# Performance work log

Hardware: AMD Instinct MI355X
Metric: run time of the kernel (lower is better)

Reference implementation:

```python
import jax, jax.numpy as jnp
import numpy as np

C = 512  # in_channels

def _maxpool2x2(t):
    # t: [B, c, H, W] -> [B, c, H//2, W//2]
    B, c, H, W = t.shape
    return t.reshape(B, c, H // 2, 2, W // 2, 2).max(axis=(3, 5))

def setup_inputs() -> dict:
    key = jax.random.key(0)
    ks = jax.random.split(key, 6)
    B, H, W = 16, 64, 64
    x = jax.random.normal(ks[0], (B, C, H, W), dtype=jnp.float32)
    # 1x1 conv weights (spectral norm is just a static rescale of the weight;
    # we model the post-normalized weight directly). Shapes: [out_c, in_c].
    scale = 0.02
    w_theta = jax.random.normal(ks[1], (C // 8, C), dtype=jnp.float32) * scale
    w_phi = jax.random.normal(ks[2], (C // 8, C), dtype=jnp.float32) * scale
    w_g = jax.random.normal(ks[3], (C // 2, C), dtype=jnp.float32) * scale
    w_o = jax.random.normal(ks[4], (C, C // 2), dtype=jnp.float32) * scale
    gamma = jnp.asarray(0.5, dtype=jnp.float32)  # nonzero so attention path matters
    return {"x": x, "w_theta": w_theta, "w_phi": w_phi, "w_g": w_g,
            "w_o": w_o, "gamma": gamma}

def reference(x, w_theta, w_phi, w_g, w_o, gamma):
    B, c, H, W = x.shape
    N = H * W
    M = N // 4
    # 1x1 convs == channel matmuls
    theta = jnp.einsum('oc,bchw->bohw', w_theta, x)            # [B, C/8, H, W]
    phi = _maxpool2x2(jnp.einsum('oc,bchw->bohw', w_phi, x))   # [B, C/8, H/2, W/2]
    g = _maxpool2x2(jnp.einsum('oc,bchw->bohw', w_g, x))       # [B, C/2, H/2, W/2]
    theta = theta.reshape(B, c // 8, N)
    phi = phi.reshape(B, c // 8, M)
    g = g.reshape(B, c // 2, M)
    # attention: softmax over keys (last dim)
    scores = jnp.einsum('bdn,bdm->bnm', theta, phi)            # [B, N, M]
    beta = jax.nn.softmax(scores, axis=-1)
    o = jnp.einsum('bvm,bnm->bvn', g, beta)                    # [B, C/2, N]
    o = o.reshape(B, c // 2, H, W)
    o = jnp.einsum('ov,bvhw->bohw', w_o, o)                    # [B, C, H, W]
    return gamma * o + x
```

## Files before the change

kernel.cpp:

```cpp
#include <hip/hip_runtime.h>
#include <hip/hip_fp16.h>

typedef unsigned int u32;
typedef unsigned short u16;
typedef u32 __attribute__((may_alias)) u32a;
typedef u16 __attribute__((may_alias)) u16a;
typedef uint4 __attribute__((may_alias)) uint4a;
typedef uint2 __attribute__((may_alias)) uint2a;
typedef float __attribute__((may_alias)) f32a;
typedef float4 __attribute__((may_alias)) float4a;

typedef __attribute__((ext_vector_type(8))) short short8v;
typedef __attribute__((ext_vector_type(4))) float float4v;

union Frag { uint4 q; short8v s; u16 u[8]; };
union F4 { float4 v; float f[4]; };

#define BATCH 16
#define CIN   512
#define NPIX  4096
#define DD    64
#define VV    256
#define MM    1024

__device__ __forceinline__ float b2f(u16 u) {
  union { u32 i; float f; } v; v.i = ((u32)u) << 16; return v.f;
}
__device__ __forceinline__ u16 f2b(float f) {
  union { float f; u32 i; } v; v.f = f;
  u32 u = v.i;
  u32 r = (u + 0x7fffu + ((u >> 16) & 1u)) >> 16;
  return (u16)r;
}
__device__ __forceinline__ u16 f2h(float f) { return __half_as_ushort(__float2half(f)); }
__device__ __forceinline__ float h2f(u16 u) { return __half2float(__ushort_as_half(u)); }

__device__ __forceinline__ u32 cvtpk(float lo, float hi) {
  u32 r;
  asm("v_cvt_pk_bf16_f32 %0, %1, %2" : "=v"(r) : "v"(lo), "v"(hi));
  return r;
}

__device__ __forceinline__ float dot2(u32 a, u32 b, float c) {
  union { u32 i; float f; } a0, a1, b0, b1;
  a0.i = a << 16; a1.i = a & 0xffff0000u;
  b0.i = b << 16; b1.i = b & 0xffff0000u;
  return fmaf(a1.f, b1.f, fmaf(a0.f, b0.f, c));
}

__global__ __launch_bounds__(256) void k_detect(const void* __restrict__ x,
                                                u32* __restrict__ meta) {
  __shared__ int bad[256];
  const int t = threadIdx.x;
  float f = b2f(((const u16a*)x)[2 * t]);
  float a = fabsf(f);
  bad[t] = (a >= 1e-6f && a <= 100.f) ? 0 : 1;
  __syncthreads();
  if (t == 0) {
    int s = 0;
#pragma unroll 16
    for (int i = 0; i < 256; ++i) s += bad[i];
    meta[0] = (s > 64) ? 1u : 0u;
  }
}

__global__ __launch_bounds__(256) void k_cvt(
    const void* __restrict__ wt, const void* __restrict__ wp,
    const void* __restrict__ wg, const void* __restrict__ wo,
    const void* __restrict__ gm, const u32* __restrict__ meta,
    u16* __restrict__ wbf, float* __restrict__ gout) {
  const int flag = (int)meta[0];
  const int i = blockIdx.x * 256 + threadIdx.x;
  const void* src; int j;
  if (i < 32768)       { src = wt; j = i; }
  else if (i < 65536)  { src = wp; j = i - 32768; }
  else if (i < 196608) { src = wg; j = i - 65536; }
  else                 { src = wo; j = i - 196608; }
  wbf[i] = flag ? f2b(((const f32a*)src)[j]) : ((const u16a*)src)[j];
  if (i == 0)
    gout[0] = flag ? ((const f32a*)gm)[0] : b2f(((const u16a*)gm)[0]);
}

__global__ __launch_bounds__(256) void k_proj(
    const void* __restrict__ x, const u16* __restrict__ w_all,
    const u32* __restrict__ meta,
    u16* __restrict__ theta, u16* __restrict__ phi_t, u16* __restrict__ g)
{
  __shared__ __align__(16) u16 xs[128][136];
  const int tid  = threadIdx.x;
  const int lane = tid & 63;
  const int wv   = tid >> 6;
  const int lg   = lane >> 4;
  const int lr   = lane & 15;
  const int blk  = blockIdx.x;
  const int b    = blk >> 5;
  const int pxt  = blk & 31;
  const int n0   = pxt * 128;
  const int rbase = wv * 96;
  const int flag = (int)meta[0];

  float4v acc[6][8];
#pragma unroll
  for (int i = 0; i < 6; ++i)
#pragma unroll
    for (int j = 0; j < 8; ++j) acc[i][j] = (float4v){0.f, 0.f, 0.f, 0.f};

  const int pg = tid & 15;
  const int cg = tid >> 4;

  for (int cc = 0; cc < 4; ++cc) {
    const int c0 = cc * 128;
    __syncthreads();
    if (flag) {
      const f32a* src = (const f32a*)x +
          ((size_t)(b * CIN + c0 + cg * 8)) * NPIX + n0 + pg * 4;
#pragma unroll
      for (int cq = 0; cq < 2; ++cq) {
        const f32a* s4 = src + (size_t)(cq * 4) * NPIX;
        F4 a0, a1, a2, a3, b0, b1, b2, b3;
        a0.v = *(const float4a*)(s4);
        b0.v = *(const float4a*)(s4 + 64);
        a1.v = *(const float4a*)(s4 + NPIX);
        b1.v = *(const float4a*)(s4 + NPIX + 64);
        a2.v = *(const float4a*)(s4 + 2 * (size_t)NPIX);
        b2.v = *(const float4a*)(s4 + 2 * (size_t)NPIX + 64);
        a3.v = *(const float4a*)(s4 + 3 * (size_t)NPIX);
        b3.v = *(const float4a*)(s4 + 3 * (size_t)NPIX + 64);
        const int colb = cg * 8 + cq * 4;
#pragma unroll
        for (int j = 0; j < 4; ++j) {
          uint2 wd; wd.x = cvtpk(a0.f[j], a1.f[j]); wd.y = cvtpk(a2.f[j], a3.f[j]);
          *(uint2a*)&xs[pg * 4 + j][colb] = wd;
          uint2 vd; vd.x = cvtpk(b0.f[j], b1.f[j]); vd.y = cvtpk(b2.f[j], b3.f[j]);
          *(uint2a*)&xs[64 + pg * 4 + j][colb] = vd;
        }
      }
    } else {
#pragma unroll 8
      for (int it = 0; it < 64; ++it) {
        int idx = tid + it * 256;
        int cl = idx >> 7, px = idx & 127;
        xs[px][cl] = ((const u16a*)x)[((size_t)(b * CIN + c0 + cl)) * NPIX + (n0 + px)];
      }
    }
    __syncthreads();

#pragma unroll
    for (int kk = 0; kk < 4; ++kk) {
      short8v bfr[8];
#pragma unroll
      for (int pt = 0; pt < 8; ++pt) {
        Frag f; f.q = *(const uint4a*)&xs[pt * 16 + lr][kk * 32 + lg * 8];
        bfr[pt] = f.s;
      }
#pragma unroll
      for (int rt = 0; rt < 6; ++rt) {
        Frag af;
        af.q = *(const uint4a*)(w_all +
            (size_t)(rbase + rt * 16 + lr) * CIN + c0 + kk * 32 + lg * 8);
#pragma unroll
        for (int pt = 0; pt < 8; ++pt)
          acc[rt][pt] = __builtin_amdgcn_mfma_f32_16x16x32_bf16(af.s, bfr[pt], acc[rt][pt], 0, 0, 0);
      }
    }
  }

#pragma unroll
  for (int rt = 0; rt < 6; ++rt) {
    const int rowb = rbase + rt * 16;
    if (rowb < 64) {
#pragma unroll
      for (int pt = 0; pt < 8; ++pt)
#pragma unroll
        for (int r = 0; r < 4; ++r) {
          int row = rowb + lg * 4 + r;
          theta[((size_t)(b * DD + row)) * NPIX + n0 + pt * 16 + lr] = f2b(acc[rt][pt][r]);
        }
    } else {
#pragma unroll
      for (int pt = 0; pt < 4; ++pt)
#pragma unroll
        for (int r = 0; r < 4; ++r) {
          int row = rowb + lg * 4 + r;
          float pm = fmaxf(acc[rt][pt][r], acc[rt][pt + 4][r]);
          float po = fmaxf(pm, __shfl_xor(pm, 1));
          if (!(lr & 1)) {
            int m = pxt * 32 + pt * 8 + (lr >> 1);
            if (row < 128) phi_t[((size_t)(b * MM + m)) * DD + (row - 64)] = f2b(po);
            else           g[((size_t)(b * VV + (row - 128))) * MM + m]    = f2b(po);
          }
        }
    }
  }
}

__global__ __launch_bounds__(512, 4) void k_attn2(
    const u16* __restrict__ theta, const u16* __restrict__ phi_t,
    const u16* __restrict__ g, u16* __restrict__ o_t)
{
  __shared__ __align__(16) u32 sc[32 * 516];
  __shared__ float pmax8[32][8];
  __shared__ float psum[32][16];
  __shared__ float sinv_s[32];

  const int tid  = threadIdx.x;
  const int lane = tid & 63;
  const int wv   = tid >> 6;
  const int lg   = lane >> 4;
  const int lr   = lane & 15;
  const int bid  = blockIdx.x;
  const int swz  = ((bid & 7) << 8) | (bid >> 3);
  const int b    = swz >> 7;
  const int bqt  = swz & 127;
  const int nq0  = bqt * 32;

  u16a* sc16 = (u16a*)sc;

  short8v qa[2][2];
#pragma unroll
  for (int qt = 0; qt < 2; ++qt)
#pragma unroll
    for (int kk = 0; kk < 2; ++kk) {
      Frag f;
#pragma unroll
      for (int i = 0; i < 8; ++i) {
        int d = kk * 32 + lg * 8 + i;
        f.u[i] = theta[((size_t)(b * DD + d)) * NPIX + nq0 + qt * 16 + lr];
      }
      qa[qt][kk] = f.s;
    }

  {
    float mx0 = -3.0e38f, mx1 = -3.0e38f;
    const u16* ptw = phi_t + ((size_t)(b * MM) + wv * 128 + lr) * DD + lg * 8;
    uint4 f0 = *(const uint4a*)(ptw);
    uint4 f1 = *(const uint4a*)(ptw + 32);
#pragma unroll
    for (int mt = 0; mt < 8; ++mt) {
      const int mtn = (mt < 7) ? mt + 1 : 7;
      uint4 n0v = *(const uint4a*)(ptw + (size_t)mtn * 16 * DD);
      uint4 n1v = *(const uint4a*)(ptw + (size_t)mtn * 16 * DD + 32);
      Frag a0; a0.q = f0; Frag a1; a1.q = f1;
      float4v s0 = {0.f, 0.f, 0.f, 0.f}, s1 = {0.f, 0.f, 0.f, 0.f};
      s0 = __builtin_amdgcn_mfma_f32_16x16x32_bf16(a0.s, qa[0][0], s0, 0, 0, 0);
      s0 = __builtin_amdgcn_mfma_f32_16x16x32_bf16(a1.s, qa[0][1], s0, 0, 0, 0);
      s1 = __builtin_amdgcn_mfma_f32_16x16x32_bf16(a0.s, qa[1][0], s1, 0, 0, 0);
      s1 = __builtin_amdgcn_mfma_f32_16x16x32_bf16(a1.s, qa[1][1], s1, 0, 0, 0);
      float c0 = fminf(fmaxf(s0[0], -6.0e4f), 6.0e4f);
      float c1 = fminf(fmaxf(s0[1], -6.0e4f), 6.0e4f);
      float c2 = fminf(fmaxf(s0[2], -6.0e4f), 6.0e4f);
      float c3 = fminf(fmaxf(s0[3], -6.0e4f), 6.0e4f);
      mx0 = fmaxf(mx0, fmaxf(fmaxf(c0, c1), fmaxf(c2, c3)));
      uint2 w0;
      w0.x = (u32)f2h(c0) | ((u32)f2h(c1) << 16);
      w0.y = (u32)f2h(c2) | ((u32)f2h(c3) << 16);
      *(uint2a*)&sc16[(size_t)lr * 1032 + wv * 128 + mt * 16 + lg * 4] = w0;
      float d0 = fminf(fmaxf(s1[0], -6.0e4f), 6.0e4f);
      float d1 = fminf(fmaxf(s1[1], -6.0e4f), 6.0e4f);
      float d2 = fminf(fmaxf(s1[2], -6.0e4f), 6.0e4f);
      float d3 = fminf(fmaxf(s1[3], -6.0e4f), 6.0e4f);
      mx1 = fmaxf(mx1, fmaxf(fmaxf(d0, d1), fmaxf(d2, d3)));
      uint2 w1;
      w1.x = (u32)f2h(d0) | ((u32)f2h(d1) << 16);
      w1.y = (u32)f2h(d2) | ((u32)f2h(d3) << 16);
      *(uint2a*)&sc16[(size_t)(16 + lr) * 1032 + wv * 128 + mt * 16 + lg * 4] = w1;
      f0 = n0v; f1 = n1v;
    }
    mx0 = fmaxf(mx0, __shfl_xor(mx0, 16));
    mx0 = fmaxf(mx0, __shfl_xor(mx0, 32));
    mx1 = fmaxf(mx1, __shfl_xor(mx1, 16));
    mx1 = fmaxf(mx1, __shfl_xor(mx1, 32));
    if (lane < 16) {
      pmax8[lr][wv]      = mx0;
      pmax8[16 + lr][wv] = mx1;
    }
  }
  __syncthreads();

  const int q  = tid & 31;
  const int sg = tid >> 5;
  {
    float maxq = pmax8[q][0];
#pragma unroll
    for (int i = 1; i < 8; ++i) maxq = fmaxf(maxq, pmax8[q][i]);
    float ssum = 0.f;
#pragma unroll 4
    for (int kp = 0; kp < 32; ++kp) {
      int kk = (kp + sg) & 31;
      int idx = q * 516 + sg * 32 + kk;
      u32 raw = sc[idx];
      float f0 = h2f((u16)(raw & 0xffffu));
      float f1 = h2f((u16)(raw >> 16));
      float e0 = __expf(fminf(f0 - maxq, 0.f));
      float e1 = __expf(fminf(f1 - maxq, 0.f));
      ssum += e0 + e1;
      sc[idx] = (u32)f2b(e0) | ((u32)f2b(e1) << 16);
    }
    psum[q][sg] = ssum;
    __syncthreads();
    float tot = 0.f;
#pragma unroll
    for (int i = 0; i < 16; ++i) tot += psum[q][i];
    if (sg == 0) sinv_s[q] = 1.f / tot;
  }
  __syncthreads();

  {
    const u16* gv0 = g + (size_t)b * (VV * MM) + ((size_t)(wv * 32) + lr) * MM + lg * 8;
    const u16* gv1 = gv0 + (size_t)16 * MM;
    const u16* p0b = sc16 + (size_t)lr * 1032 + lg * 8;
    const u16* p1b = p0b + (size_t)16 * 1032;

    float4v a00 = {0.f,0.f,0.f,0.f}, a01 = {0.f,0.f,0.f,0.f};
    float4v a10 = {0.f,0.f,0.f,0.f}, a11 = {0.f,0.f,0.f,0.f};

    uint4 ga0 = *(const uint4a*)(gv0);
    uint4 ga1 = *(const uint4a*)(gv1);
    uint4 pa0 = *(const uint4a*)(p0b);
    uint4 pa1 = *(const uint4a*)(p1b);
    uint4 gb0 = *(const uint4a*)(gv0 + 32);
    uint4 gb1 = *(const uint4a*)(gv1 + 32);
    uint4 pb0 = *(const uint4a*)(p0b + 32);
    uint4 pb1 = *(const uint4a*)(p1b + 32);

#pragma unroll 4
    for (int ms = 0; ms < 32; ms += 2) {
      const int m2 = (ms + 2 < 32) ? ms + 2 : 30;
      const int m3 = (ms + 3 < 32) ? ms + 3 : 31;
      uint4 gc0 = *(const uint4a*)(gv0 + m2 * 32);
      uint4 gc1 = *(const uint4a*)(gv1 + m2 * 32);
      uint4 pc0 = *(const uint4a*)(p0b + m2 * 32);
      uint4 pc1 = *(const uint4a*)(p1b + m2 * 32);
      {
        Frag x0, x1, y0, y1; x0.q = ga0; x1.q = ga1; y0.q = pa0; y1.q = pa1;
        a00 = __builtin_amdgcn_mfma_f32_16x16x32_bf16(x0.s, y0.s, a00, 0, 0, 0);
        a01 = __builtin_amdgcn_mfma_f32_16x16x32_bf16(x0.s, y1.s, a01, 0, 0, 0);
        a10 = __builtin_amdgcn_mfma_f32_16x16x32_bf16(x1.s, y0.s, a10, 0, 0, 0);
        a11 = __builtin_amdgcn_mfma_f32_16x16x32_bf16(x1.s, y1.s, a11, 0, 0, 0);
      }
      uint4 gd0 = *(const uint4a*)(gv0 + m3 * 32);
      uint4 gd1 = *(const uint4a*)(gv1 + m3 * 32);
      uint4 pd0 = *(const uint4a*)(p0b + m3 * 32);
      uint4 pd1 = *(const uint4a*)(p1b + m3 * 32);
      {
        Frag x0, x1, y0, y1; x0.q = gb0; x1.q = gb1; y0.q = pb0; y1.q = pb1;
        a00 = __builtin_amdgcn_mfma_f32_16x16x32_bf16(x0.s, y0.s, a00, 0, 0, 0);
        a01 = __builtin_amdgcn_mfma_f32_16x16x32_bf16(x0.s, y1.s, a01, 0, 0, 0);
        a10 = __builtin_amdgcn_mfma_f32_16x16x32_bf16(x1.s, y0.s, a10, 0, 0, 0);
        a11 = __builtin_amdgcn_mfma_f32_16x16x32_bf16(x1.s, y1.s, a11, 0, 0, 0);
      }
      ga0 = gc0; ga1 = gc1; pa0 = pc0; pa1 = pc1;
      gb0 = gd0; gb1 = gd1; pb0 = pd0; pb1 = pd1;
    }

    const float si0 = sinv_s[lr];
    const float si1 = sinv_s[16 + lr];
    {
      uint2 wd;
      wd.x = cvtpk(a00[0] * si0, a00[1] * si0);
      wd.y = cvtpk(a00[2] * si0, a00[3] * si0);
      *(uint2a*)(o_t + ((size_t)(b * NPIX + nq0 + lr)) * VV + wv * 32 + lg * 4) = wd;
      wd.x = cvtpk(a01[0] * si1, a01[1] * si1);
      wd.y = cvtpk(a01[2] * si1, a01[3] * si1);
      *(uint2a*)(o_t + ((size_t)(b * NPIX + nq0 + 16 + lr)) * VV + wv * 32 + lg * 4) = wd;
      wd.x = cvtpk(a10[0] * si0, a10[1] * si0);
      wd.y = cvtpk(a10[2] * si0, a10[3] * si0);
      *(uint2a*)(o_t + ((size_t)(b * NPIX + nq0 + lr)) * VV + wv * 32 + 16 + lg * 4) = wd;
      wd.x = cvtpk(a11[0] * si1, a11[1] * si1);
      wd.y = cvtpk(a11[2] * si1, a11[3] * si1);
      *(uint2a*)(o_t + ((size_t)(b * NPIX + nq0 + 16 + lr)) * VV + wv * 32 + 16 + lg * 4) = wd;
    }
  }
}

__global__ __launch_bounds__(256) void k_oproj(
    const u16* __restrict__ o_t, const u16* __restrict__ wo,
    const void* __restrict__ x, const float* __restrict__ gamma_p,
    const u32* __restrict__ meta, void* __restrict__ out)
{
  __shared__ __align__(16) u16 os[64][264];
  const int tid  = threadIdx.x;
  const int lane = tid & 63;
  const int wv   = tid >> 6;
  const int lg   = lane >> 4;
  const int lr   = lane & 15;
  const int bid  = blockIdx.x;
  const int swz  = ((bid & 7) << 7) | (bid >> 3);
  const int b    = swz >> 6;
  const int nt   = swz & 63;
  const int n0   = nt * 64;
  const int flag = (int)meta[0];

#pragma unroll
  for (int it = 0; it < 8; ++it) {
    int idx = tid + it * 256;
    int row = idx >> 5, cq = idx & 31;
    *(uint4a*)&os[row][cq * 8] =
        *(const uint4a*)(o_t + ((size_t)(b * NPIX + n0 + row)) * VV + cq * 8);
  }
  __syncthreads();

  float4v acc[8][4];
#pragma unroll
  for (int i = 0; i < 8; ++i)
#pragma unroll
    for (int j = 0; j < 4; ++j) acc[i][j] = (float4v){0.f, 0.f, 0.f, 0.f};

#pragma unroll
  for (int kk = 0; kk < 8; ++kk) {
    short8v bf4[4];
#pragma unroll
    for (int pt = 0; pt < 4; ++pt) {
      Frag f; f.q = *(const uint4a*)&os[pt * 16 + lr][kk * 32 + lg * 8];
      bf4[pt] = f.s;
    }
#pragma unroll
    for (int rt = 0; rt < 8; ++rt) {
      Frag af;
      af.q = *(const uint4a*)(wo + (size_t)(wv * 128 + rt * 16 + lr) * VV + kk * 32 + lg * 8);
#pragma unroll
      for (int pt = 0; pt < 4; ++pt)
        acc[rt][pt] = __builtin_amdgcn_mfma_f32_16x16x32_bf16(af.s, bf4[pt], acc[rt][pt], 0, 0, 0);
    }
  }

  const float gmv = gamma_p[0];
#pragma unroll
  for (int rt = 0; rt < 8; ++rt) {
#pragma unroll
    for (int pt = 0; pt < 4; ++pt) {
#pragma unroll
      for (int r = 0; r < 4; ++r) {
        int oc = wv * 128 + rt * 16 + lg * 4 + r;
        size_t off = ((size_t)(b * CIN + oc)) * NPIX + n0 + pt * 16 + lr;
        if (flag) {
          ((f32a*)out)[off] = gmv * acc[rt][pt][r] + ((const f32a*)x)[off];
        } else {
          ((u16a*)out)[off] = f2b(gmv * acc[rt][pt][r] + b2f(((const u16a*)x)[off]));
        }
      }
    }
  }
}

__global__ __launch_bounds__(256) void k_attn(
    const u16* __restrict__ theta, const u16* __restrict__ phi_t,
    const u16* __restrict__ g, const u16* __restrict__ wo,
    const void* __restrict__ x, const float* __restrict__ gamma_p,
    const u32* __restrict__ meta, void* __restrict__ out)
{
  __shared__ __align__(16) u32 sc[16 * 516];
  __shared__ __align__(16) u16 ot[16 * 264];
  __shared__ float pmax[16][16];
  __shared__ float psum[16][16];
  __shared__ float sinv_s[16];

  const int tid  = threadIdx.x;
  const int lane = tid & 63;
  const int wv   = tid >> 6;
  const int lg   = lane >> 4;
  const int lr   = lane & 15;
  const int blk  = blockIdx.x;
  const int b    = blk >> 8;
  const int qt   = blk & 255;
  const int nq0  = qt * 16;
  const int flag = (int)meta[0];

  u16a* sc16 = (u16a*)sc;

  short8v qa[2];
#pragma unroll
  for (int kk = 0; kk < 2; ++kk) {
    Frag f;
#pragma unroll
    for (int i = 0; i < 8; ++i) {
      int d = kk * 32 + lg * 8 + i;
      f.u[i] = theta[((size_t)(b * DD + d)) * NPIX + nq0 + lr];
    }
    qa[kk] = f.s;
  }

  {
    const u16* pt = phi_t + (size_t)b * (MM * DD);
#pragma unroll 2
    for (int mt = 0; mt < 16; ++mt) {
      const int m0 = wv * 256 + mt * 16;
      float4v s = {0.f, 0.f, 0.f, 0.f};
#pragma unroll
      for (int kk = 0; kk < 2; ++kk) {
        Frag f; f.q = *(const uint4a*)(pt + (size_t)(m0 + lr) * DD + kk * 32 + lg * 8);
        s = __builtin_amdgcn_mfma_f32_16x16x32_bf16(qa[kk], f.s, s, 0, 0, 0);
      }
#pragma unroll
      for (int r = 0; r < 4; ++r) {
        int qq = lg * 4 + r;
        float v = fminf(fmaxf(s[r], -6.0e4f), 6.0e4f);
        sc16[qq * 1032 + m0 + lr] = f2h(v);
      }
    }
  }
  __syncthreads();

  {
    const int q  = tid & 15;
    const int sg = tid >> 4;
    float mx = -3.0e38f;
#pragma unroll 8
    for (int k = 0; k < 64; ++k) {
      int kk = (k + sg * 2) & 63;
      mx = fmaxf(mx, h2f(sc16[q * 1032 + sg * 64 + kk]));
    }
    pmax[q][sg] = mx;
    __syncthreads();
    float maxq = -3.0e38f;
#pragma unroll
    for (int i = 0; i < 16; ++i) maxq = fmaxf(maxq, pmax[q][i]);
    float ssum = 0.f;
#pragma unroll 4
    for (int kp = 0; kp < 32; ++kp) {
      int kk = (kp + sg) & 31;
      int idx = q * 516 + sg * 32 + kk;
      u32 raw = sc[idx];
      float f0 = h2f((u16)(raw & 0xffffu));
      float f1 = h2f((u16)(raw >> 16));
      float e0 = __expf(fminf(f0 - maxq, 0.f));
      float e1 = __expf(fminf(f1 - maxq, 0.f));
      ssum += e0 + e1;
      sc[idx] = (u32)f2b(e0) | ((u32)f2b(e1) << 16);
    }
    psum[q][sg] = ssum;
    __syncthreads();
    float tot = 0.f;
#pragma unroll
    for (int i = 0; i < 16; ++i) tot += psum[q][i];
    if (sg == 0) sinv_s[q] = 1.f / tot;
  }
  __syncthreads();

  const int q  = tid & 15;
  const int sg = tid >> 4;
  {
    float4v oacc[4];
#pragma unroll
    for (int i = 0; i < 4; ++i) oacc[i] = (float4v){0.f, 0.f, 0.f, 0.f};
    const u16* gb = g + (size_t)b * (VV * MM);
#pragma unroll 2
    for (int ms = 0; ms < 32; ++ms) {
      Frag pf; pf.q = *(const uint4a*)(sc16 + lr * 1032 + ms * 32 + lg * 8);
#pragma unroll
      for (int vt = 0; vt < 4; ++vt) {
        Frag gf; gf.q = *(const uint4a*)(gb + (size_t)(wv * 64 + vt * 16 + lr) * MM + ms * 32 + lg * 8);
        oacc[vt] = __builtin_amdgcn_mfma_f32_16x16x32_bf16(gf.s, pf.s, oacc[vt], 0, 0, 0);
      }
    }
    const float si = sinv_s[lr];
#pragma unroll
    for (int vt = 0; vt < 4; ++vt) {
      u32 lo = (u32)f2b(oacc[vt][0] * si) | ((u32)f2b(oacc[vt][1] * si) << 16);
      u32 hi = (u32)f2b(oacc[vt][2] * si) | ((u32)f2b(oacc[vt][3] * si) << 16);
      u32a* p = (u32a*)&ot[lr * 264 + wv * 64 + vt * 16 + lg * 4];
      p[0] = lo; p[1] = hi;
    }
  }
  __syncthreads();

  {
    short8v ob[8];
#pragma unroll
    for (int ks = 0; ks < 8; ++ks) {
      Frag f; f.q = *(const uint4a*)(ot + lr * 264 + ks * 32 + lg * 8);
      ob[ks] = f.s;
    }
    const float gmv = gamma_p[0];
    const int oc0 = wv * 128;
#pragma unroll 2
    for (int oct = 0; oct < 8; ++oct) {
      float4v c = {0.f, 0.f, 0.f, 0.f};
#pragma unroll
      for (int ks = 0; ks < 8; ++ks) {
        Frag f; f.q = *(const uint4a*)(wo + (size_t)(oc0 + oct * 16 + lr) * VV + ks * 32 + lg * 8);
        c = __builtin_amdgcn_mfma_f32_16x16x32_bf16(f.s, ob[ks], c, 0, 0, 0);
      }
#pragma unroll
      for (int r = 0; r < 4; ++r) {
        int oc = oc0 + oct * 16 + lg * 4 + r;
        size_t off = ((size_t)(b * CIN + oc)) * NPIX + nq0 + lr;
        if (flag) {
          ((f32a*)out)[off] = gmv * c[r] + ((const f32a*)x)[off];
        } else {
          ((u16a*)out)[off] = f2b(gmv * c[r] + b2f(((const u16a*)x)[off]));
        }
      }
    }
  }
}

extern "C" void kernel_launch(void* const* d_in, const int* in_sizes, int n_in,
                              void* d_out, int out_size, void* d_ws, size_t ws_size,
                              hipStream_t stream) {
  (void)in_sizes; (void)n_in; (void)out_size;
  const void* x  = d_in[0];
  const void* wt = d_in[1];
  const void* wp = d_in[2];
  const void* wg = d_in[3];
  const void* wo = d_in[4];
  const void* gm = d_in[5];

  u16* theta = (u16*)d_ws;
  u16* phi_t = theta + (size_t)BATCH * DD * NPIX;
  u16* g     = phi_t + (size_t)BATCH * MM * DD;
  u16* wbf   = g     + (size_t)BATCH * VV * MM;
  float* gamma_f = (float*)(wbf + 327680);
  u32* meta      = (u32*)(gamma_f + 1);
  u16* o_t   = (u16*)d_ws + 9764896;
  const size_t need = ((size_t)9764896 + (size_t)BATCH * NPIX * VV) * 2;

  hipLaunchKernelGGL(k_detect, dim3(1), dim3(256), 0, stream, x, meta);
  hipLaunchKernelGGL(k_cvt, dim3(1280), dim3(256), 0, stream,
                     wt, wp, wg, wo, gm, meta, wbf, gamma_f);
  hipLaunchKernelGGL(k_proj, dim3(BATCH * 32), dim3(256), 0, stream,
                     x, wbf, meta, theta, phi_t, g);
  if (ws_size >= need) {
    hipLaunchKernelGGL(k_attn2, dim3(BATCH * 128), dim3(512), 0, stream,
                       theta, phi_t, g, o_t);
    hipLaunchKernelGGL(k_oproj, dim3(BATCH * 64), dim3(256), 0, stream,
                       o_t, wbf + 196608, x, gamma_f, meta, d_out);
  } else {
    hipLaunchKernelGGL(k_attn, dim3(BATCH * 256), dim3(256), 0, stream,
                       theta, phi_t, g, wbf + 196608, x, gamma_f, meta, d_out);
  }
}
```

Baseline: 636.9 us.

## Retile output projection into smaller LDS-free tiles with vectorized epilogue

Rewrites k_oproj so each block covers 32 pixels by 256 output channels instead of 64 pixels by 512 channels, launching four times as many blocks. The shared-memory staging of o_t is removed, so operands are read straight from global memory. The MFMA operand roles are swapped so the accumulator layout gives four contiguous pixels per lane, which lets the epilogue read x and write out with float4 or uint2 accesses instead of scalar ones. The aim is higher occupancy, fewer registers, and coalesced residual I/O. The cost is more redundant global and cache reads of o_t and the weights across blocks.

```diff
diff --git a/kernel.cpp b/kernel.cpp
--- a/kernel.cpp
+++ b/kernel.cpp
@@ -373,71 +373,77 @@
   }
 }
 
-__global__ __launch_bounds__(256) void k_oproj(
+__global__ __launch_bounds__(256, 4) void k_oproj(
     const u16* __restrict__ o_t, const u16* __restrict__ wo,
     const void* __restrict__ x, const float* __restrict__ gamma_p,
     const u32* __restrict__ meta, void* __restrict__ out)
 {
-  __shared__ __align__(16) u16 os[64][264];
   const int tid  = threadIdx.x;
   const int lane = tid & 63;
   const int wv   = tid >> 6;
   const int lg   = lane >> 4;
   const int lr   = lane & 15;
   const int bid  = blockIdx.x;
-  const int swz  = ((bid & 7) << 7) | (bid >> 3);
-  const int b    = swz >> 6;
-  const int nt   = swz & 63;
-  const int n0   = nt * 64;
+  const int swz  = ((bid & 7) << 9) | (bid >> 3);
+  const int b    = swz >> 8;
+  const int nt   = (swz >> 1) & 127;
+  const int och  = swz & 1;
+  const int n0   = nt * 32;
+  const int ocb  = och * 256 + wv * 64;
   const int flag = (int)meta[0];
 
-#pragma unroll
-  for (int it = 0; it < 8; ++it) {
-    int idx = tid + it * 256;
-    int row = idx >> 5, cq = idx & 31;
-    *(uint4a*)&os[row][cq * 8] =
-        *(const uint4a*)(o_t + ((size_t)(b * NPIX + n0 + row)) * VV + cq * 8);
-  }
-  __syncthreads();
-
-  float4v acc[8][4];
-#pragma unroll
-  for (int i = 0; i < 8; ++i)
-#pragma unroll
-    for (int j = 0; j < 4; ++j) acc[i][j] = (float4v){0.f, 0.f, 0.f, 0.f};
-
-#pragma unroll
+  float4v acc[4][2];
+#pragma unroll
+  for (int j = 0; j < 4; ++j)
+#pragma unroll
+    for (int t = 0; t < 2; ++t) acc[j][t] = (float4v){0.f, 0.f, 0.f, 0.f};
+
+  const u16* obl = o_t + ((size_t)(b * NPIX) + n0 + lr) * VV;
+  const u16* wbl = wo + (size_t)(ocb + lr) * VV;
+
+#pragma unroll 2
   for (int kk = 0; kk < 8; ++kk) {
-    short8v bf4[4];
-#pragma unroll
-    for (int pt = 0; pt < 4; ++pt) {
-      Frag f; f.q = *(const uint4a*)&os[pt * 16 + lr][kk * 32 + lg * 8];
-      bf4[pt] = f.s;
-    }
-#pragma unroll
-    for (int rt = 0; rt < 8; ++rt) {
-      Frag af;
-      af.q = *(const uint4a*)(wo + (size_t)(wv * 128 + rt * 16 + lr) * VV + kk * 32 + lg * 8);
-#pragma unroll
-      for (int pt = 0; pt < 4; ++pt)
-        acc[rt][pt] = __builtin_amdgcn_mfma_f32_16x16x32_bf16(af.s, bf4[pt], acc[rt][pt], 0, 0, 0);
-    }
+    const int ko = kk * 32 + lg * 8;
+    Frag a0, a1, w0, w1, w2, w3;
+    a0.q = *(const uint4a*)(obl + ko);
+    a1.q = *(const uint4a*)(obl + (size_t)16 * VV + ko);
+    w0.q = *(const uint4a*)(wbl + ko);
+    w1.q = *(const uint4a*)(wbl + (size_t)16 * VV + ko);
+    w2.q = *(const uint4a*)(wbl + (size_t)32 * VV + ko);
+    w3.q = *(const uint4a*)(wbl + (size_t)48 * VV + ko);
+    acc[0][0] = __builtin_amdgcn_mfma_f32_16x16x32_bf16(a0.s, w0.s, acc[0][0], 0, 0, 0);
+    acc[0][1] = __builtin_amdgcn_mfma_f32_16x16x32_bf16(a1.s, w0.s, acc[0][1], 0, 0, 0);
+    acc[1][0] = __builtin_amdgcn_mfma_f32_16x16x32_bf16(a0.s, w1.s, acc[1][0], 0, 0, 0);
+    acc[1][1] = __builtin_amdgcn_mfma_f32_16x16x32_bf16(a1.s, w1.s, acc[1][1], 0, 0, 0);
+    acc[2][0] = __builtin_amdgcn_mfma_f32_16x16x32_bf16(a0.s, w2.s, acc[2][0], 0, 0, 0);
+    acc[2][1] = __builtin_amdgcn_mfma_f32_16x16x32_bf16(a1.s, w2.s, acc[2][1], 0, 0, 0);
+    acc[3][0] = __builtin_amdgcn_mfma_f32_16x16x32_bf16(a0.s, w3.s, acc[3][0], 0, 0, 0);
+    acc[3][1] = __builtin_amdgcn_mfma_f32_16x16x32_bf16(a1.s, w3.s, acc[3][1], 0, 0, 0);
   }
 
   const float gmv = gamma_p[0];
 #pragma unroll
-  for (int rt = 0; rt < 8; ++rt) {
-#pragma unroll
-    for (int pt = 0; pt < 4; ++pt) {
-#pragma unroll
-      for (int r = 0; r < 4; ++r) {
-        int oc = wv * 128 + rt * 16 + lg * 4 + r;
-        size_t off = ((size_t)(b * CIN + oc)) * NPIX + n0 + pt * 16 + lr;
-        if (flag) {
-          ((f32a*)out)[off] = gmv * acc[rt][pt][r] + ((const f32a*)x)[off];
-        } else {
-          ((u16a*)out)[off] = f2b(gmv * acc[rt][pt][r] + b2f(((const u16a*)x)[off]));
-        }
+  for (int j = 0; j < 4; ++j) {
+    const int oc = ocb + j * 16 + lr;
+#pragma unroll
+    for (int t = 0; t < 2; ++t) {
+      const size_t off = ((size_t)(b * CIN + oc)) * NPIX + n0 + t * 16 + lg * 4;
+      if (flag) {
+        F4 xv; xv.v = *(const float4a*)((const f32a*)x + off);
+        F4 o;
+        o.f[0] = gmv * acc[j][t][0] + xv.f[0];
+        o.f[1] = gmv * acc[j][t][1] + xv.f[1];
+        o.f[2] = gmv * acc[j][t][2] + xv.f[2];
+        o.f[3] = gmv * acc[j][t][3] + xv.f[3];
+        *(float4a*)((f32a*)out + off) = o.v;
+      } else {
+        uint2 xv = *(const uint2a*)((const u16a*)x + off);
+        uint2 st;
+        st.x = (u32)f2b(gmv * acc[j][t][0] + b2f((u16)(xv.x & 0xffffu))) |
+               ((u32)f2b(gmv * acc[j][t][1] + b2f((u16)(xv.x >> 16))) << 16);
+        st.y = (u32)f2b(gmv * acc[j][t][2] + b2f((u16)(xv.y & 0xffffu))) |
+               ((u32)f2b(gmv * acc[j][t][3] + b2f((u16)(xv.y >> 16))) << 16);
+        *(uint2a*)((u16a*)out + off) = st;
       }
     }
   }
@@ -623,7 +629,7 @@
   if (ws_size >= need) {
     hipLaunchKernelGGL(k_attn2, dim3(BATCH * 128), dim3(512), 0, stream,
                        theta, phi_t, g, o_t);
-    hipLaunchKernelGGL(k_oproj, dim3(BATCH * 64), dim3(256), 0, stream,
+    hipLaunchKernelGGL(k_oproj, dim3(BATCH * 256), dim3(256), 0, stream,
                        o_t, wbf + 196608, x, gamma_f, meta, d_out);
   } else {
     hipLaunchKernelGGL(k_attn, dim3(BATCH * 256), dim3(256), 0, stream,
```

Result: faster. 570.2 us (-10.5%).
